# Kernel optimization log

Hardware: AMD Instinct MI355X
Metric: run time of the kernel (lower is better)

Reference implementation:

```python
import jax, jax.numpy as jnp
import numpy as np

H = 1024        # hidden_size
V = 50257       # output_size (vocab)
L = 50          # max_length (encoder positions)
N_LAYERS = 2    # python loop count over the shared single-layer GRU


def setup_inputs() -> dict:
    key = jax.random.key(0)
    ks = jax.random.split(key, 16)
    s = 0.02
    return {
        "input_ids": jax.random.randint(ks[0], (1,), 0, V),
        "hidden": jax.random.normal(ks[1], (1, 1, H), jnp.float32),
        "encoder_outputs": jax.random.normal(ks[2], (L, H), jnp.float32),
        # learned parameters
        "emb": jax.random.normal(ks[3], (V, H), jnp.float32) * s,
        "attn_w": jax.random.normal(ks[4], (L, 2 * H), jnp.float32) * s,
        "attn_b": jnp.zeros((L,), jnp.float32),
        "comb_w": jax.random.normal(ks[5], (H, 2 * H), jnp.float32) * s,
        "comb_b": jnp.zeros((H,), jnp.float32),
        "w_ih": jax.random.normal(ks[6], (3 * H, H), jnp.float32) * s,
        "w_hh": jax.random.normal(ks[7], (3 * H, H), jnp.float32) * s,
        "b_ih": jnp.zeros((3 * H,), jnp.float32),
        "b_hh": jnp.zeros((3 * H,), jnp.float32),
        "out_w": jax.random.normal(ks[8], (V, H), jnp.float32) * s,
        "out_b": jnp.zeros((V,), jnp.float32),
    }


def _gru_cell(x, h, w_ih, w_hh, b_ih, b_hh):
    # PyTorch GRU gate order: [r, z, n] stacked along dim 0 of (3H, H) weights.
    gx = w_ih @ x + b_ih
    gh = w_hh @ h + b_hh
    r = jax.nn.sigmoid(gx[:H] + gh[:H])
    z = jax.nn.sigmoid(gx[H:2 * H] + gh[H:2 * H])
    n = jnp.tanh(gx[2 * H:] + r * gh[2 * H:])
    return (1.0 - z) * n + z * h


def reference(input_ids, hidden, encoder_outputs, emb, attn_w, attn_b,
              comb_w, comb_b, w_ih, w_hh, b_ih, b_hh, out_w, out_b):
    # batch=1 single decode step; dropout is identity (eval mode)
    embedded = emb[input_ids[0]]                     # [H]
    h = hidden[0, 0]                                 # [H]
    concat = jnp.concatenate([embedded, h])          # [2H]
    attn_weights = jax.nn.softmax(attn_w @ concat + attn_b)   # [L]
    attn_applied = attn_weights @ encoder_outputs    # [H]  (bmm with batch 1)
    output = comb_w @ jnp.concatenate([embedded, attn_applied]) + comb_b  # [H]
    for _ in range(N_LAYERS):                        # shared-weight GRU called twice
        x = jax.nn.relu(output)
        h = _gru_cell(x, h, w_ih, w_hh, b_ih, b_hh)
        output = h
    log_probs = jax.nn.log_softmax(out_w @ output + out_b)    # [V]
    return log_probs[None, :], h[None, None, :], attn_weights[None, :]
```

## Files before the change

kernel.cpp:

```cpp
#include <hip/hip_runtime.h>
#include <hip/hip_bf16.h>

#define H 1024
#define V 50257
#define L 50

__global__ void scores_kernel(const int* __restrict__ input_ids,
                              const float* __restrict__ hidden,
                              const float* __restrict__ emb,
                              const float* __restrict__ attn_w,
                              const float* __restrict__ attn_b,
                              float* __restrict__ ws_scores) {
    __shared__ float s_part[8];
    const int tid = threadIdx.x;
    const int l   = blockIdx.x;
    const int wave = tid >> 6, lane = tid & 63;
    const int token = input_ids[0];

    float4 a = ((const float4*)(attn_w + (size_t)l * 2 * H))[tid];
    float4 x = (tid < 256) ? ((const float4*)(emb + (size_t)token * H))[tid]
                           : ((const float4*)hidden)[tid - 256];
    float acc = a.x * x.x + a.y * x.y + a.z * x.z + a.w * x.w;
    #pragma unroll
    for (int off = 32; off; off >>= 1) acc += __shfl_down(acc, off);
    if (lane == 0) s_part[wave] = acc;
    __syncthreads();
    if (tid == 0) {
        float s = 0.f;
        #pragma unroll
        for (int w = 0; w < 8; ++w) s += s_part[w];
        ws_scores[l] = s + attn_b[l];
    }
}

__global__ void applied_kernel(const float* __restrict__ ws_scores,
                               const float* __restrict__ enc,
                               float* __restrict__ ws_app,
                               float* __restrict__ out_attnw) {
    const int j = blockIdx.x * 256 + threadIdx.x;
    float w[L];
    float m = ws_scores[0];
    #pragma unroll
    for (int l = 1; l < L; ++l) m = fmaxf(m, ws_scores[l]);
    float s = 0.f;
    #pragma unroll
    for (int l = 0; l < L; ++l) { w[l] = expf(ws_scores[l] - m); s += w[l]; }
    float inv = 1.f / s;
    float acc = 0.f;
    #pragma unroll
    for (int l = 0; l < L; ++l) { w[l] *= inv; acc += w[l] * enc[l * H + j]; }
    ws_app[j] = acc;
    if (blockIdx.x == 0 && threadIdx.x < L) out_attnw[threadIdx.x] = w[threadIdx.x];
}

__global__ void comb_kernel(const float* __restrict__ comb_w,
                            const float* __restrict__ comb_b,
                            const int* __restrict__ input_ids,
                            const float* __restrict__ emb,
                            const float* __restrict__ applied,
                            float* __restrict__ x1) {
    __shared__ __align__(16) float s_c[2 * H];
    const int tid = threadIdx.x;
    const int token = input_ids[0];
    ((float4*)s_c)[tid] = ((const float4*)(emb + (size_t)token * H))[tid];
    ((float4*)(s_c + H))[tid] = ((const float4*)applied)[tid];
    __syncthreads();

    const int wave = tid >> 6, lane = tid & 63;
    const int i = blockIdx.x * 4 + wave;
    const float4* r4 = (const float4*)(comb_w + (size_t)i * 2 * H);
    const float4* c4 = (const float4*)s_c;
    float acc = 0.f;
    #pragma unroll
    for (int kk = 0; kk < 8; ++kk) {
        int k = kk * 64 + lane;
        float4 a = r4[k], b = c4[k];
        acc += a.x * b.x + a.y * b.y + a.z * b.z + a.w * b.w;
    }
    #pragma unroll
    for (int off = 32; off; off >>= 1) acc += __shfl_down(acc, off);
    if (lane == 0) x1[i] = fmaxf(acc + comb_b[i], 0.f);
}

__global__ void gru_kernel(const float* __restrict__ x,
                           const float* __restrict__ hprev,
                           const float* __restrict__ w_ih,
                           const float* __restrict__ w_hh,
                           const float* __restrict__ b_ih,
                           const float* __restrict__ b_hh,
                           float* __restrict__ h_out,
                           float* __restrict__ x_out,
                           float* __restrict__ h_copy)
{
    __shared__ __align__(16) float s_x[H];
    __shared__ __align__(16) float s_h[H];
    const int tid = threadIdx.x;
    ((float4*)s_x)[tid] = ((const float4*)x)[tid];
    ((float4*)s_h)[tid] = ((const float4*)hprev)[tid];
    __syncthreads();

    const int wave = tid >> 6, lane = tid & 63;
    const int i = blockIdx.x * 4 + wave;
    const float4* x4 = (const float4*)s_x;
    const float4* h4 = (const float4*)s_h;
    const float4* wr_x = (const float4*)(w_ih + (size_t)i * H);
    const float4* wz_x = (const float4*)(w_ih + (size_t)(H + i) * H);
    const float4* wn_x = (const float4*)(w_ih + (size_t)(2 * H + i) * H);
    const float4* wr_h = (const float4*)(w_hh + (size_t)i * H);
    const float4* wz_h = (const float4*)(w_hh + (size_t)(H + i) * H);
    const float4* wn_h = (const float4*)(w_hh + (size_t)(2 * H + i) * H);

    float ar = 0.f, az = 0.f, an = 0.f, br = 0.f, bz = 0.f, bn = 0.f;
    #pragma unroll
    for (int kk = 0; kk < 4; ++kk) {
        int k = kk * 64 + lane;
        float4 xv = x4[k], hv = h4[k], t;
        t = wr_x[k]; ar += t.x * xv.x + t.y * xv.y + t.z * xv.z + t.w * xv.w;
        t = wz_x[k]; az += t.x * xv.x + t.y * xv.y + t.z * xv.z + t.w * xv.w;
        t = wn_x[k]; an += t.x * xv.x + t.y * xv.y + t.z * xv.z + t.w * xv.w;
        t = wr_h[k]; br += t.x * hv.x + t.y * hv.y + t.z * hv.z + t.w * hv.w;
        t = wz_h[k]; bz += t.x * hv.x + t.y * hv.y + t.z * hv.z + t.w * hv.w;
        t = wn_h[k]; bn += t.x * hv.x + t.y * hv.y + t.z * hv.z + t.w * hv.w;
    }
    #pragma unroll
    for (int off = 32; off; off >>= 1) {
        ar += __shfl_down(ar, off); az += __shfl_down(az, off);
        an += __shfl_down(an, off); br += __shfl_down(br, off);
        bz += __shfl_down(bz, off); bn += __shfl_down(bn, off);
    }
    if (lane == 0) {
        float gxr = ar + b_ih[i],         ghr = br + b_hh[i];
        float gxz = az + b_ih[H + i],     ghz = bz + b_hh[H + i];
        float gxn = an + b_ih[2 * H + i], ghn = bn + b_hh[2 * H + i];
        float r = 1.f / (1.f + expf(-(gxr + ghr)));
        float z = 1.f / (1.f + expf(-(gxz + ghz)));
        float n = tanhf(gxn + r * ghn);
        float hn = (1.f - z) * n + z * s_h[i];
        h_out[i] = hn;
        if (x_out)  x_out[i]  = fmaxf(hn, 0.f);
        if (h_copy) h_copy[i] = hn;
    }
}

__global__ void logits_kernel(const float* __restrict__ out_w,
                              const float* __restrict__ out_b,
                              const float* __restrict__ h,
                              float* __restrict__ out,
                              float* __restrict__ partials) {
    __shared__ __align__(16) float s_h[H];
    __shared__ float s_part[4];
    const int tid = threadIdx.x;
    ((float4*)s_h)[tid] = ((const float4*)h)[tid];
    __syncthreads();

    const int wave = tid >> 6, lane = tid & 63;
    const float4* h4 = (const float4*)s_h;
    const int v0 = blockIdx.x * 8 + wave * 2;
    const int v1 = v0 + 1;
    float acc0 = 0.f, acc1 = 0.f;
    const float4* w0 = (const float4*)(out_w + (size_t)v0 * H);
    const float4* w1 = (const float4*)(out_w + (size_t)v1 * H);
    if (v1 < V) {
        #pragma unroll
        for (int kk = 0; kk < 4; ++kk) {
            int k = kk * 64 + lane;
            float4 b = h4[k];
            float4 a0 = w0[k], a1 = w1[k];
            acc0 += a0.x * b.x + a0.y * b.y + a0.z * b.z + a0.w * b.w;
            acc1 += a1.x * b.x + a1.y * b.y + a1.z * b.z + a1.w * b.w;
        }
    } else if (v0 < V) {
        #pragma unroll
        for (int kk = 0; kk < 4; ++kk) {
            int k = kk * 64 + lane;
            float4 b = h4[k];
            float4 a0 = w0[k];
            acc0 += a0.x * b.x + a0.y * b.y + a0.z * b.z + a0.w * b.w;
        }
    }
    #pragma unroll
    for (int off = 32; off; off >>= 1) {
        acc0 += __shfl_down(acc0, off);
        acc1 += __shfl_down(acc1, off);
    }
    float psum = 0.f;
    if (lane == 0) {
        if (v0 < V) { float lg = acc0 + out_b[v0]; out[v0] = lg; psum += expf(lg); }
        if (v1 < V) { float lg = acc1 + out_b[v1]; out[v1] = lg; psum += expf(lg); }
        s_part[wave] = psum;
    }
    __syncthreads();
    if (tid == 0)
        partials[blockIdx.x] = s_part[0] + s_part[1] + s_part[2] + s_part[3];
}

__global__ void lse_kernel(const float* __restrict__ partials, int n,
                           float* __restrict__ lse) {
    __shared__ float red[256];
    const int tid = threadIdx.x;
    float s = 0.f;
    for (int i = tid; i < n; i += 256) s += partials[i];
    red[tid] = s;
    __syncthreads();
    for (int off = 128; off; off >>= 1) {
        if (tid < off) red[tid] += red[tid + off];
        __syncthreads();
    }
    if (tid == 0) *lse = logf(red[0]);
}

__global__ void sub_kernel(float* __restrict__ out,
                           const float* __restrict__ lse) {
    const int v = blockIdx.x * 256 + threadIdx.x;
    if (v < V) out[v] -= *lse;
}

extern "C" void kernel_launch(void* const* d_in, const int* in_sizes, int n_in,
                              void* d_out, int out_size, void* d_ws, size_t ws_size,
                              hipStream_t stream) {
    const int*   input_ids = (const int*)d_in[0];
    const float* hidden    = (const float*)d_in[1];
    const float* enc       = (const float*)d_in[2];
    const float* emb       = (const float*)d_in[3];
    const float* attn_w    = (const float*)d_in[4];
    const float* attn_b    = (const float*)d_in[5];
    const float* comb_w    = (const float*)d_in[6];
    const float* comb_b    = (const float*)d_in[7];
    const float* w_ih      = (const float*)d_in[8];
    const float* w_hh      = (const float*)d_in[9];
    const float* b_ih      = (const float*)d_in[10];
    const float* b_hh      = (const float*)d_in[11];
    const float* out_w     = (const float*)d_in[12];
    const float* out_b     = (const float*)d_in[13];

    float* out = (float*)d_out;
    float* ws  = (float*)d_ws;
    float* ws_scores = ws;
    float* ws_app    = ws + 64;
    float* ws_x1     = ws_app + H;
    float* ws_h1     = ws_x1 + H;
    float* ws_x2     = ws_h1 + H;
    float* ws_h2     = ws_x2 + H;
    float* ws_part   = ws_h2 + H;
    float* ws_lse    = ws_part + 6400;

    const int nblk_logits = (V + 7) / 8;

    scores_kernel<<<L, 512, 0, stream>>>(input_ids, hidden, emb, attn_w, attn_b,
                                         ws_scores);
    applied_kernel<<<4, 256, 0, stream>>>(ws_scores, enc, ws_app, out + V + H);
    comb_kernel<<<256, 256, 0, stream>>>(comb_w, comb_b, input_ids, emb, ws_app,
                                         ws_x1);
    gru_kernel<<<256, 256, 0, stream>>>(ws_x1, hidden, w_ih, w_hh, b_ih, b_hh,
                                        ws_h1, ws_x2, nullptr);
    gru_kernel<<<256, 256, 0, stream>>>(ws_x2, ws_h1, w_ih, w_hh, b_ih, b_hh,
                                        ws_h2, nullptr, out + V);
    logits_kernel<<<nblk_logits, 256, 0, stream>>>(out_w, out_b, ws_h2,
                                                   out, ws_part);
    lse_kernel<<<1, 256, 0, stream>>>(ws_part, nblk_logits, ws_lse);
    sub_kernel<<<(V + 255) / 256, 256, 0, stream>>>(out, ws_lse);
}
```

Measured before the change: 430.9 us.

## Fuse all decoder stages into one cooperative persistent kernel with grid syncs

Replaces the chain of separate kernel launches (scores, attention apply, combine, two GRU steps, logits, log-softmax) with a single cooperative kernel of 256 blocks x 512 threads that separates stages with grid.sync. This removes per-launch overhead and inter-kernel gaps, which dominate for this small batch-1 decode. The cost is grid-wide barriers and fewer blocks for the large out_w GEMV. The old multi-kernel path remains as a fallback if the cooperative launch fails.

```diff
diff --git a/kernel.cpp b/kernel.cpp
--- a/kernel.cpp
+++ b/kernel.cpp
@@ -1,9 +1,216 @@
 #include <hip/hip_runtime.h>
-#include <hip/hip_bf16.h>
+#include <hip/hip_cooperative_groups.h>
 
 #define H 1024
 #define V 50257
 #define L 50
+
+namespace cg = cooperative_groups;
+
+
+__device__ __forceinline__ float wave_reduce(float v) {
+    #pragma unroll
+    for (int off = 32; off; off >>= 1) v += __shfl_down(v, off);
+    return v;
+}
+
+__device__ __forceinline__ float dot4(float4 a, float4 b) {
+    return a.x * b.x + a.y * b.y + a.z * b.z + a.w * b.w;
+}
+
+struct FusedArgs {
+    const int*   input_ids;
+    const float* hidden;
+    const float* enc;
+    const float* emb;
+    const float* attn_w;
+    const float* attn_b;
+    const float* comb_w;
+    const float* comb_b;
+    const float* w_ih;
+    const float* w_hh;
+    const float* b_ih;
+    const float* b_hh;
+    const float* out_w;
+    const float* out_b;
+    float*       out;
+    float*       ws;
+};
+
+__global__ void __launch_bounds__(512, 2) fused_kernel(FusedArgs a) {
+    __shared__ __align__(16) float s_c[2 * H];
+    __shared__ __align__(16) float s_x[H];
+    __shared__ __align__(16) float s_h[H];
+    __shared__ float s_g[4][6];
+    __shared__ float s_part[8];
+    __shared__ float s_red[256];
+
+    cg::grid_group grid = cg::this_grid();
+    const int tid  = threadIdx.x;
+    const int bid  = blockIdx.x;
+    const int wave = tid >> 6, lane = tid & 63;
+
+    float* ws_scores = a.ws;
+    float* ws_app    = a.ws + 64;
+    float* ws_x1     = ws_app + H;
+    float* ws_h1     = ws_x1 + H;
+    float* ws_x2     = ws_h1 + H;
+    float* ws_h2     = ws_x2 + H;
+    float* ws_part   = ws_h2 + H;
+
+    const int token = a.input_ids[0];
+
+    if (bid < L) {
+        float4 aw = ((const float4*)(a.attn_w + (size_t)bid * 2 * H))[tid];
+        float4 xv = (tid < 256) ? ((const float4*)(a.emb + (size_t)token * H))[tid]
+                                : ((const float4*)a.hidden)[tid - 256];
+        float acc = wave_reduce(dot4(aw, xv));
+        if (lane == 0) s_part[wave] = acc;
+        __syncthreads();
+        if (tid == 0) {
+            float s = 0.f;
+            #pragma unroll
+            for (int w = 0; w < 8; ++w) s += s_part[w];
+            ws_scores[bid] = s + a.attn_b[bid];
+        }
+    }
+    grid.sync();
+
+    if (bid < 2) {
+        const int j = bid * 512 + tid;
+        float m = ws_scores[0];
+        #pragma unroll
+        for (int l = 1; l < L; ++l) m = fmaxf(m, ws_scores[l]);
+        float ssum = 0.f;
+        #pragma unroll
+        for (int l = 0; l < L; ++l) ssum += expf(ws_scores[l] - m);
+        float inv = 1.f / ssum;
+        float acc = 0.f;
+        #pragma unroll
+        for (int l = 0; l < L; ++l) {
+            float wl = expf(ws_scores[l] - m);
+            wl *= inv;
+            acc += wl * a.enc[l * H + j];
+        }
+        ws_app[j] = acc;
+        if (bid == 0 && tid < L) {
+            float wl = expf(ws_scores[tid] - m);
+            a.out[V + H + tid] = wl * inv;
+        }
+    }
+    grid.sync();
+
+    if (tid < 256) ((float4*)s_c)[tid]           = ((const float4*)(a.emb + (size_t)token * H))[tid];
+    else           ((float4*)(s_c + H))[tid - 256] = ((const float4*)ws_app)[tid - 256];
+    __syncthreads();
+    if (wave < 4) {
+        const int i = bid * 4 + wave;
+        const float4* r4 = (const float4*)(a.comb_w + (size_t)i * 2 * H);
+        const float4* c4 = (const float4*)s_c;
+        float acc = 0.f;
+        #pragma unroll
+        for (int kk = 0; kk < 8; ++kk) {
+            int k = kk * 64 + lane;
+            acc += dot4(r4[k], c4[k]);
+        }
+        acc = wave_reduce(acc);
+        if (lane == 0) ws_x1[i] = fmaxf(acc + a.comb_b[i], 0.f);
+    }
+    grid.sync();
+
+    for (int layer = 0; layer < 2; ++layer) {
+        const float* xg = layer ? ws_x2 : ws_x1;
+        const float* hg = layer ? ws_h1 : a.hidden;
+        if (tid < 256) ((float4*)s_x)[tid]       = ((const float4*)xg)[tid];
+        else           ((float4*)s_h)[tid - 256] = ((const float4*)hg)[tid - 256];
+        __syncthreads();
+        #pragma unroll
+        for (int q = 0; q < 3; ++q) {
+            const int t = wave * 3 + q;
+            const int r = t / 6, g = t % 6;
+            const int i = bid * 4 + r;
+            const float4* w4 = (const float4*)((g < 3)
+                ? (a.w_ih + (size_t)(g * H + i) * H)
+                : (a.w_hh + (size_t)((g - 3) * H + i) * H));
+            const float4* v4 = (const float4*)((g < 3) ? s_x : s_h);
+            float acc = 0.f;
+            #pragma unroll
+            for (int kk = 0; kk < 4; ++kk) {
+                int k = kk * 64 + lane;
+                acc += dot4(w4[k], v4[k]);
+            }
+            acc = wave_reduce(acc);
+            if (lane == 0) s_g[r][g] = acc;
+        }
+        __syncthreads();
+        if (tid < 4) {
+            const int r = tid, i = bid * 4 + r;
+            float gxr = s_g[r][0] + a.b_ih[i];         float ghr = s_g[r][3] + a.b_hh[i];
+            float gxz = s_g[r][1] + a.b_ih[H + i];     float ghz = s_g[r][4] + a.b_hh[H + i];
+            float gxn = s_g[r][2] + a.b_ih[2 * H + i]; float ghn = s_g[r][5] + a.b_hh[2 * H + i];
+            float rr = 1.f / (1.f + expf(-(gxr + ghr)));
+            float zz = 1.f / (1.f + expf(-(gxz + ghz)));
+            float nn = tanhf(gxn + rr * ghn);
+            float hn = (1.f - zz) * nn + zz * s_h[i];
+            if (layer == 0) { ws_h1[i] = hn; ws_x2[i] = fmaxf(hn, 0.f); }
+            else            { ws_h2[i] = hn; a.out[V + i] = hn; }
+        }
+        grid.sync();
+    }
+
+    {
+        const float4* h4 = (const float4*)ws_h2;
+        const float4 hv0 = h4[lane];
+        const float4 hv1 = h4[64 + lane];
+        const float4 hv2 = h4[128 + lane];
+        const float4 hv3 = h4[192 + lane];
+        float psum = 0.f;
+        for (int pass = 0; pass < 7; ++pass) {
+            const int v0 = pass * 8192 + bid * 32 + wave * 4;
+            if (v0 >= V) continue;
+            #pragma unroll
+            for (int r = 0; r < 4; ++r) {
+                const int v  = v0 + r;
+                const int vc = (v < V) ? v : (V - 1);
+                const float4* w4 = (const float4*)(a.out_w + (size_t)vc * H);
+                float acc = 0.f;
+                acc += dot4(w4[lane], hv0);
+                acc += dot4(w4[64 + lane], hv1);
+                acc += dot4(w4[128 + lane], hv2);
+                acc += dot4(w4[192 + lane], hv3);
+                acc = wave_reduce(acc);
+                if (lane == 0 && v < V) {
+                    float lg = acc + a.out_b[v];
+                    a.out[v] = lg;
+                    psum += expf(lg);
+                }
+            }
+        }
+        if (lane == 0) s_part[wave] = psum;
+        __syncthreads();
+        if (tid == 0) {
+            float s = 0.f;
+            #pragma unroll
+            for (int w = 0; w < 8; ++w) s += s_part[w];
+            ws_part[bid] = s;
+        }
+    }
+    grid.sync();
+
+    s_red[tid & 255] = 0.f;
+    __syncthreads();
+    if (tid < 256) s_red[tid] = ws_part[tid];
+    __syncthreads();
+    #pragma unroll
+    for (int off = 128; off; off >>= 1) {
+        if (tid < off) s_red[tid] += s_red[tid + off];
+        __syncthreads();
+    }
+    const float lse = logf(s_red[0]);
+    const int v = bid * 512 + tid;
+    if (v < V) a.out[v] -= lse;
+}
+
 
 __global__ void scores_kernel(const int* __restrict__ input_ids,
                               const float* __restrict__ hidden,
@@ -90,8 +297,7 @@
                            const float* __restrict__ b_hh,
                            float* __restrict__ h_out,
                            float* __restrict__ x_out,
-                           float* __restrict__ h_copy)
-{
+                           float* __restrict__ h_copy) {
     __shared__ __align__(16) float s_x[H];
     __shared__ __align__(16) float s_h[H];
     const int tid = threadIdx.x;
@@ -235,6 +441,16 @@
 
     float* out = (float*)d_out;
     float* ws  = (float*)d_ws;
+
+    FusedArgs args = { input_ids, hidden, enc, emb, attn_w, attn_b,
+                       comb_w, comb_b, w_ih, w_hh, b_ih, b_hh,
+                       out_w, out_b, out, ws };
+    void* kp[] = { &args };
+    hipError_t err = hipLaunchCooperativeKernel((void*)fused_kernel,
+                                                dim3(256), dim3(512),
+                                                kp, 0, stream);
+    if (err == hipSuccess) return;
+
     float* ws_scores = ws;
     float* ws_app    = ws + 64;
     float* ws_x1     = ws_app + H;
```

New measurement: 588.4 us. 36.5% more time.

## Fuse attention/combine head into one kernel and merge LSE with subtraction

Applied to the files above, without the earlier changes.

Replaces the scores, applied and combine kernels with one head kernel. Every block recomputes the 50 attention scores, the softmax and the attention-applied vector redundantly, then computes its four rows of the combine matvec. The single-block LSE reduction is folded into the subtraction kernel, so each of its ~197 blocks re-reduces the ~6.3K partials itself. The aim is to drop three kernel launches and their serial gaps, paid for with redundant reads of attn_w and enc in every block.

```diff
diff --git a/kernel.cpp b/kernel.cpp
--- a/kernel.cpp
+++ b/kernel.cpp
@@ -1,85 +1,92 @@
 #include <hip/hip_runtime.h>
-#include <hip/hip_bf16.h>
 
 #define H 1024
 #define V 50257
 #define L 50
 
-__global__ void scores_kernel(const int* __restrict__ input_ids,
-                              const float* __restrict__ hidden,
-                              const float* __restrict__ emb,
-                              const float* __restrict__ attn_w,
-                              const float* __restrict__ attn_b,
-                              float* __restrict__ ws_scores) {
-    __shared__ float s_part[8];
-    const int tid = threadIdx.x;
-    const int l   = blockIdx.x;
+
+__device__ __forceinline__ float wave_reduce(float v) {
+    #pragma unroll
+    for (int off = 32; off; off >>= 1) v += __shfl_down(v, off);
+    return v;
+}
+
+__device__ __forceinline__ float dot4(float4 a, float4 b) {
+    return a.x * b.x + a.y * b.y + a.z * b.z + a.w * b.w;
+}
+
+__global__ void __launch_bounds__(512) head_kernel(
+        const int* __restrict__ input_ids,
+        const float* __restrict__ hidden,
+        const float* __restrict__ enc,
+        const float* __restrict__ emb,
+        const float* __restrict__ attn_w,
+        const float* __restrict__ attn_b,
+        const float* __restrict__ comb_w,
+        const float* __restrict__ comb_b,
+        float* __restrict__ out_attnw,
+        float* __restrict__ ws_x1) {
+    __shared__ __align__(16) float s_cat[2 * H];
+    __shared__ float s_sc[64];
+
+    const int tid  = threadIdx.x;
+    const int bid  = blockIdx.x;
     const int wave = tid >> 6, lane = tid & 63;
     const int token = input_ids[0];
 
-    float4 a = ((const float4*)(attn_w + (size_t)l * 2 * H))[tid];
-    float4 x = (tid < 256) ? ((const float4*)(emb + (size_t)token * H))[tid]
-                           : ((const float4*)hidden)[tid - 256];
-    float acc = a.x * x.x + a.y * x.y + a.z * x.z + a.w * x.w;
-    #pragma unroll
-    for (int off = 32; off; off >>= 1) acc += __shfl_down(acc, off);
-    if (lane == 0) s_part[wave] = acc;
-    __syncthreads();
-    if (tid == 0) {
-        float s = 0.f;
-        #pragma unroll
-        for (int w = 0; w < 8; ++w) s += s_part[w];
-        ws_scores[l] = s + attn_b[l];
-    }
-}
-
-__global__ void applied_kernel(const float* __restrict__ ws_scores,
-                               const float* __restrict__ enc,
-                               float* __restrict__ ws_app,
-                               float* __restrict__ out_attnw) {
-    const int j = blockIdx.x * 256 + threadIdx.x;
-    float w[L];
-    float m = ws_scores[0];
-    #pragma unroll
-    for (int l = 1; l < L; ++l) m = fmaxf(m, ws_scores[l]);
-    float s = 0.f;
-    #pragma unroll
-    for (int l = 0; l < L; ++l) { w[l] = expf(ws_scores[l] - m); s += w[l]; }
-    float inv = 1.f / s;
-    float acc = 0.f;
-    #pragma unroll
-    for (int l = 0; l < L; ++l) { w[l] *= inv; acc += w[l] * enc[l * H + j]; }
-    ws_app[j] = acc;
-    if (blockIdx.x == 0 && threadIdx.x < L) out_attnw[threadIdx.x] = w[threadIdx.x];
-}
-
-__global__ void comb_kernel(const float* __restrict__ comb_w,
-                            const float* __restrict__ comb_b,
-                            const int* __restrict__ input_ids,
-                            const float* __restrict__ emb,
-                            const float* __restrict__ applied,
-                            float* __restrict__ x1) {
-    __shared__ __align__(16) float s_c[2 * H];
-    const int tid = threadIdx.x;
-    const int token = input_ids[0];
-    ((float4*)s_c)[tid] = ((const float4*)(emb + (size_t)token * H))[tid];
-    ((float4*)(s_c + H))[tid] = ((const float4*)applied)[tid];
-    __syncthreads();
-
-    const int wave = tid >> 6, lane = tid & 63;
-    const int i = blockIdx.x * 4 + wave;
-    const float4* r4 = (const float4*)(comb_w + (size_t)i * 2 * H);
-    const float4* c4 = (const float4*)s_c;
-    float acc = 0.f;
-    #pragma unroll
-    for (int kk = 0; kk < 8; ++kk) {
-        int k = kk * 64 + lane;
-        float4 a = r4[k], b = c4[k];
-        acc += a.x * b.x + a.y * b.y + a.z * b.z + a.w * b.w;
-    }
-    #pragma unroll
-    for (int off = 32; off; off >>= 1) acc += __shfl_down(acc, off);
-    if (lane == 0) x1[i] = fmaxf(acc + comb_b[i], 0.f);
+    ((float4*)s_cat)[tid] = (tid < 256)
+        ? ((const float4*)(emb + (size_t)token * H))[tid]
+        : ((const float4*)hidden)[tid - 256];
+    __syncthreads();
+
+    for (int l = wave; l < L; l += 8) {
+        const float4* w4 = (const float4*)(attn_w + (size_t)l * 2 * H);
+        const float4* c4 = (const float4*)s_cat;
+        float acc = 0.f;
+        #pragma unroll
+        for (int kk = 0; kk < 8; ++kk) {
+            int k = kk * 64 + lane;
+            acc += dot4(w4[k], c4[k]);
+        }
+        acc = wave_reduce(acc);
+        if (lane == 0) s_sc[l] = acc + attn_b[l];
+    }
+    __syncthreads();
+
+    {
+        float m = s_sc[0];
+        #pragma unroll
+        for (int l = 1; l < L; ++l) m = fmaxf(m, s_sc[l]);
+        float ssum = 0.f;
+        #pragma unroll
+        for (int l = 0; l < L; ++l) ssum += expf(s_sc[l] - m);
+        float inv = 1.f / ssum;
+        float acc0 = 0.f, acc1 = 0.f;
+        #pragma unroll
+        for (int l = 0; l < L; ++l) {
+            float wl = expf(s_sc[l] - m) * inv;
+            acc0 += wl * enc[l * H + tid];
+            acc1 += wl * enc[l * H + 512 + tid];
+        }
+        if (bid == 0 && tid < L) out_attnw[tid] = expf(s_sc[tid] - m) * inv;
+        s_cat[H + tid]       = acc0;
+        s_cat[H + 512 + tid] = acc1;
+    }
+    __syncthreads();
+
+    if (wave < 4) {
+        const int i = bid * 4 + wave;
+        const float4* r4 = (const float4*)(comb_w + (size_t)i * 2 * H);
+        const float4* c4 = (const float4*)s_cat;
+        float acc = 0.f;
+        #pragma unroll
+        for (int kk = 0; kk < 8; ++kk) {
+            int k = kk * 64 + lane;
+            acc += dot4(r4[k], c4[k]);
+        }
+        acc = wave_reduce(acc);
+        if (lane == 0) ws_x1[i] = fmaxf(acc + comb_b[i], 0.f);
+    }
 }
 
 __global__ void gru_kernel(const float* __restrict__ x,
@@ -194,8 +201,8 @@
         partials[blockIdx.x] = s_part[0] + s_part[1] + s_part[2] + s_part[3];
 }
 
-__global__ void lse_kernel(const float* __restrict__ partials, int n,
-                           float* __restrict__ lse) {
+__global__ void sublse_kernel(const float* __restrict__ partials, int n,
+                              float* __restrict__ out) {
     __shared__ float red[256];
     const int tid = threadIdx.x;
     float s = 0.f;
@@ -206,13 +213,9 @@
         if (tid < off) red[tid] += red[tid + off];
         __syncthreads();
     }
-    if (tid == 0) *lse = logf(red[0]);
-}
-
-__global__ void sub_kernel(float* __restrict__ out,
-                           const float* __restrict__ lse) {
-    const int v = blockIdx.x * 256 + threadIdx.x;
-    if (v < V) out[v] -= *lse;
+    const float lse = logf(red[0]);
+    const int v = blockIdx.x * 256 + tid;
+    if (v < V) out[v] -= lse;
 }
 
 extern "C" void kernel_launch(void* const* d_in, const int* in_sizes, int n_in,
@@ -235,28 +238,23 @@
 
     float* out = (float*)d_out;
     float* ws  = (float*)d_ws;
-    float* ws_scores = ws;
-    float* ws_app    = ws + 64;
-    float* ws_x1     = ws_app + H;
+    float* ws_x1     = ws;
     float* ws_h1     = ws_x1 + H;
     float* ws_x2     = ws_h1 + H;
     float* ws_h2     = ws_x2 + H;
     float* ws_part   = ws_h2 + H;
-    float* ws_lse    = ws_part + 6400;
 
     const int nblk_logits = (V + 7) / 8;
 
-    scores_kernel<<<L, 512, 0, stream>>>(input_ids, hidden, emb, attn_w, attn_b,
-                                         ws_scores);
-    applied_kernel<<<4, 256, 0, stream>>>(ws_scores, enc, ws_app, out + V + H);
-    comb_kernel<<<256, 256, 0, stream>>>(comb_w, comb_b, input_ids, emb, ws_app,
-                                         ws_x1);
+    head_kernel<<<256, 512, 0, stream>>>(input_ids, hidden, enc, emb,
+                                         attn_w, attn_b, comb_w, comb_b,
+                                         out + V + H, ws_x1);
     gru_kernel<<<256, 256, 0, stream>>>(ws_x1, hidden, w_ih, w_hh, b_ih, b_hh,
                                         ws_h1, ws_x2, nullptr);
     gru_kernel<<<256, 256, 0, stream>>>(ws_x2, ws_h1, w_ih, w_hh, b_ih, b_hh,
                                         ws_h2, nullptr, out + V);
     logits_kernel<<<nblk_logits, 256, 0, stream>>>(out_w, out_b, ws_h2,
                                                    out, ws_part);
-    lse_kernel<<<1, 256, 0, stream>>>(ws_part, nblk_logits, ws_lse);
-    sub_kernel<<<(V + 255) / 256, 256, 0, stream>>>(out, ws_lse);
-}
+    sublse_kernel<<<(V + 255) / 256, 256, 0, stream>>>(ws_part, nblk_logits,
+                                                       out);
+}
```

Result: no change. 435.6 us (+1.1%).
